# Kernel optimization log

Hardware: AMD Instinct MI355X
Metric: run time of the kernel (lower is better)

Reference implementation:

```python
import jax, jax.numpy as jnp
import numpy as np

N_USERS = 50000
N_ENTITIES = 100000
N_NODES = N_USERS + N_ENTITIES
N_EDGES = 3000000
EMB_DIM = 64
WEIGHT_SIZES = [64, 64, 32, 16]  # [emb_dim] + weight_size
BATCH = 8192
LEAKY_SLOPE = 0.2  # KGAT (TF reference) uses leaky_relu alpha=0.2
EPS = 1e-12


def setup_inputs() -> dict:
    key = jax.random.key(0)
    ks = jax.random.split(key, 24)
    inp = {}
    inp["users"] = jax.random.randint(ks[0], (BATCH,), 0, N_USERS, dtype=jnp.int32)
    inp["pos_items"] = jax.random.randint(ks[1], (BATCH,), 0, N_ENTITIES, dtype=jnp.int32)
    inp["neg_items"] = jax.random.randint(ks[2], (BATCH,), 0, N_ENTITIES, dtype=jnp.int32)
    inp["all_h"] = jax.random.randint(ks[3], (N_EDGES,), 0, N_NODES, dtype=jnp.int32)
    inp["all_t"] = jax.random.randint(ks[4], (N_EDGES,), 0, N_NODES, dtype=jnp.int32)
    inp["A_values"] = jax.random.uniform(ks[5], (N_EDGES,), dtype=jnp.float32)
    inp["user_embed"] = jax.random.normal(ks[6], (N_USERS, EMB_DIM), dtype=jnp.float32) * 0.1
    inp["entity_embed"] = jax.random.normal(ks[7], (N_ENTITIES, EMB_DIM), dtype=jnp.float32) * 0.1
    ki = 8
    for k in range(3):
        din, dout = WEIGHT_SIZES[k], WEIGHT_SIZES[k + 1]
        scale = float(np.sqrt(2.0 / (din + dout)))  # xavier-ish
        inp[f"W_gc_{k}"] = jax.random.normal(ks[ki], (din, dout), dtype=jnp.float32) * scale; ki += 1
        inp[f"b_gc_{k}"] = jax.random.normal(ks[ki], (1, dout), dtype=jnp.float32) * scale; ki += 1
        inp[f"W_bi_{k}"] = jax.random.normal(ks[ki], (din, dout), dtype=jnp.float32) * scale; ki += 1
        inp[f"b_bi_{k}"] = jax.random.normal(ks[ki], (1, dout), dtype=jnp.float32) * scale; ki += 1
    return inp


def _bi_interaction(ego, all_h, all_t, A_values, layers, n_nodes):
    # KGAT bi-interaction aggregator over edge-list sparse adjacency.
    outs = [ego]
    for (W_gc, b_gc, W_bi, b_bi) in layers:
        # sparse A @ ego : gather tails, weight by attention, scatter-add to heads
        msgs = A_values[:, None] * ego[all_t]                       # [E, d]
        side = jax.ops.segment_sum(msgs, all_h, num_segments=n_nodes)  # [N, d]
        sum_emb = jax.nn.leaky_relu((ego + side) @ W_gc + b_gc, negative_slope=LEAKY_SLOPE)
        bi_emb = jax.nn.leaky_relu((ego * side) @ W_bi + b_bi, negative_slope=LEAKY_SLOPE)
        ego = sum_emb + bi_emb
        norm = ego / jnp.maximum(jnp.linalg.norm(ego, axis=1, keepdims=True), EPS)
        outs.append(norm)
    return jnp.concatenate(outs, axis=1)  # [N, 64+64+32+16]


def reference(users, pos_items, neg_items, all_h, all_t, A_values,
              user_embed, entity_embed,
              W_gc_0, b_gc_0, W_bi_0, b_bi_0,
              W_gc_1, b_gc_1, W_bi_1, b_bi_1,
              W_gc_2, b_gc_2, W_bi_2, b_bi_2):
    n_users = user_embed.shape[0]
    n_nodes = n_users + entity_embed.shape[0]
    ego = jnp.concatenate([user_embed, entity_embed], axis=0)  # [N, 64]
    layers = [(W_gc_0, b_gc_0, W_bi_0, b_bi_0),
              (W_gc_1, b_gc_1, W_bi_1, b_bi_1),
              (W_gc_2, b_gc_2, W_bi_2, b_bi_2)]
    all_emb = _bi_interaction(ego, all_h, all_t, A_values, layers, n_nodes)
    ua, ea = all_emb[:n_users], all_emb[n_users:]
    u_e = ua[users]
    pos_i_e = ea[pos_items]
    neg_i_e = ea[neg_items]
    return (u_e, pos_i_e, neg_i_e)
```

## Files before the change

### kernel.cpp

```cpp
#include <hip/hip_runtime.h>
#include <math.h>

#define N_USERS    50000
#define N_ENTITIES 100000
#define N_NODES    150000
#define N_EDGES    3000000
#define BATCH      8192
#define SLOPE      0.2f
#define EPSF       1e-12f

#define NBUK   2344
#define CAP    1536
#define STR    2560
#define PADM   16
#define BLK_E  12288
#define NPB    ((N_EDGES + BLK_E - 1) / BLK_E)
#define PBLK   1024
#define EPT    (BLK_E / PBLK)
#define CH     4096
#define PFW    (NBUK + 1)
#define CASTB  ((N_NODES * 64 / 4 + PBLK - 1) / PBLK)

__device__ __forceinline__ unsigned f2bf(float f) {
    unsigned u = __float_as_uint(f);
    return (u + 0x7FFFu + ((u >> 16) & 1u)) >> 16;
}
__device__ __forceinline__ float bf_lo(unsigned d) { return __uint_as_float(d << 16); }
__device__ __forceinline__ float bf_hi(unsigned d) { return __uint_as_float(d); }

__global__ __launch_bounds__(PBLK)
void prep_k(const int* __restrict__ all_h, const int* __restrict__ all_t,
            const float* __restrict__ A,
            int* __restrict__ prefix, int2* __restrict__ rec_src,
            const float* __restrict__ user_emb, const float* __restrict__ ent_emb,
            unsigned short* __restrict__ ego0_bf) {
    __shared__ int pos[NBUK];
    __shared__ int wsum[PBLK / 64];
    __shared__ int2 srec[CH];

    int t = threadIdx.x;

    if (blockIdx.x >= NPB) {
        int idx = (blockIdx.x - NPB) * PBLK + t;
        const int total = N_NODES * 64 / 4;
        if (idx >= total) return;
        int ge = idx * 4;
        const float* src = (ge < N_USERS * 64) ? user_emb + ge
                                               : ent_emb + (ge - N_USERS * 64);
        float4 v = *(const float4*)src;
        ushort4 o;
        o.x = (unsigned short)f2bf(v.x);
        o.y = (unsigned short)f2bf(v.y);
        o.z = (unsigned short)f2bf(v.z);
        o.w = (unsigned short)f2bf(v.w);
        *(ushort4*)(ego0_bf + ge) = o;
        return;
    }

    for (int i = t; i < NBUK; i += PBLK) pos[i] = 0;
    __syncthreads();

    int e0 = blockIdx.x * BLK_E;
    int e1 = e0 + BLK_E; if (e1 > N_EDGES) e1 = N_EDGES;
    int tot = e1 - e0;

    int h[EPT]; int tt[EPT]; float aa[EPT];
    #pragma unroll
    for (int k = 0; k < EPT; ++k) {
        int e = e0 + k * PBLK + t;
        bool v = e < e1;
        h[k]  = v ? all_h[e] : -1;
        tt[k] = v ? all_t[e] : 0;
        aa[k] = v ? A[e] : 0.f;
    }
    #pragma unroll
    for (int k = 0; k < EPT; ++k)
        if (h[k] >= 0) atomicAdd(&pos[h[k] >> 6], 1);
    __syncthreads();

    int c[3];
    int i0 = t * 3;
    int tsum = 0;
    #pragma unroll
    for (int j = 0; j < 3; ++j) {
        int idx = i0 + j;
        c[j] = (idx < NBUK) ? pos[idx] : 0;
        tsum += c[j];
    }

    int lane = t & 63, w = t >> 6;
    int incl = tsum;
    #pragma unroll
    for (int off = 1; off < 64; off <<= 1) {
        int x = __shfl_up(incl, off, 64);
        if (lane >= off) incl += x;
    }
    if (lane == 63) wsum[w] = incl;
    __syncthreads();
    int wbase = 0;
    for (int j = 0; j < w; ++j) wbase += wsum[j];
    int excl = wbase + (incl - tsum);

    size_t prow = (size_t)blockIdx.x * PFW;
    #pragma unroll
    for (int j = 0; j < 3; ++j) {
        int idx = i0 + j;
        if (idx < NBUK) { pos[idx] = excl; prefix[prow + idx] = excl; }
        excl += c[j];
    }
    if (t == PBLK - 1) prefix[prow + NBUK] = excl;
    __syncthreads();

    int pp[EPT];
    #pragma unroll
    for (int k = 0; k < EPT; ++k)
        pp[k] = (h[k] >= 0) ? atomicAdd(&pos[h[k] >> 6], 1) : -1;

    for (int base = 0; base < tot; base += CH) {
        __syncthreads();
        int lim = tot - base; if (lim > CH) lim = CH;
        #pragma unroll
        for (int k = 0; k < EPT; ++k) {
            int s = pp[k] - base;
            if (s >= 0 && s < CH)
                srec[s] = make_int2(tt[k] | ((h[k] & 63) << 18), __float_as_int(aa[k]));
        }
        __syncthreads();
        const int4* s4 = (const int4*)srec;
        int4* d4 = (int4*)(rec_src + e0 + base);
        int lim2 = lim >> 1;
        for (int s = t; s < lim2; s += PBLK) d4[s] = s4[s];
    }
}

__global__ __launch_bounds__(256)
void local_sort_k(const int* __restrict__ prefix, const int2* __restrict__ rec_src,
                  int2* __restrict__ rec, int2* __restrict__ range) {
    __shared__ int2 sin[CAP];
    __shared__ int2 sout[STR];
    __shared__ int cnt64[64];
    __shared__ int pos64[64];
    __shared__ int sc[256];
    __shared__ int s_ptot;
    int b = blockIdx.x, t = threadIdx.x;

    if (t < 64) cnt64[t] = 0;

    int rstart = 0, n_t = 0;
    if (t < NPB) {
        const int* prow = prefix + (size_t)t * PFW + b;
        int s0 = prow[0];
        int s1 = prow[1];
        rstart = t * BLK_E + s0;
        n_t = s1 - s0;
    }
    sc[t] = n_t;
    __syncthreads();

    for (int off = 1; off < 256; off <<= 1) {
        int v = sc[t];
        int u = (t >= off) ? sc[t - off] : 0;
        __syncthreads();
        sc[t] = v + u;
        __syncthreads();
    }
    int cnt = sc[255]; if (cnt > CAP) cnt = CAP;

    if (t < NPB && n_t > 0) {
        int d = sc[t] - n_t;
        for (int j = 0; j < n_t; ++j) {
            int dj = d + j;
            if (dj >= CAP) break;
            int2 p = rec_src[rstart + j];
            sin[dj] = p;
            atomicAdd(&cnt64[(p.x >> 18) & 63], 1);
        }
    }
    __syncthreads();

    if (t < 64) {
        int v = cnt64[t];
        int pv = (v + PADM - 1) & ~(PADM - 1);
        int sum = pv;
        #pragma unroll
        for (int off = 1; off < 64; off <<= 1) {
            int x = __shfl_up(sum, off, 64);
            if (t >= off) sum += x;
        }
        pos64[t] = sum - pv;
        if (t == 63) s_ptot = sum;
    }
    __syncthreads();
    int ptot = s_ptot;

    for (int i = t; i < ptot; i += 256) sout[i] = make_int2(0, 0);
    __syncthreads();

    for (int i = t; i < cnt; i += 256) {
        int2 p = sin[i];
        int l = (p.x >> 18) & 63;
        int dst = atomicAdd(&pos64[l], 1);
        sout[dst] = make_int2(p.x & 0x3FFFF, p.y);
    }
    __syncthreads();

    for (int i = t; i < ptot; i += 256)
        rec[(size_t)b * STR + i] = sout[i];

    if (t < 64) {
        int v = cnt64[t];
        int pv = (v + PADM - 1) & ~(PADM - 1);
        int sum = pv;
        #pragma unroll
        for (int off = 1; off < 64; off <<= 1) {
            int x = __shfl_up(sum, off, 64);
            if (t >= off) sum += x;
        }
        int start = b * STR + (sum - pv);
        int node = b * 64 + t;
        if (node < N_NODES) range[node] = make_int2(start, start + pv);
    }
}

template<int DIN>
__global__ __launch_bounds__(256)
void side_k(const int2* __restrict__ range, const int2* __restrict__ rec,
            const unsigned short* __restrict__ tab, float* __restrict__ side) {
    constexpr int LPR = DIN / 8;
    constexpr int EPW = 64 / LPR;

    int w = threadIdx.x >> 6;
    int lane = threadIdx.x & 63;
    int h = blockIdx.x * 4 + w;

    int2 rg = range[h];
    int e0 = rg.x, e1 = rg.y;
    int g = lane / LPR;
    int q = lane % LPR;

    float acc[8];
    #pragma unroll
    for (int j = 0; j < 8; ++j) acc[j] = 0.f;

    int e = e0;
    for (; e + 2 * EPW <= e1; e += 2 * EPW) {
        int2 p0 = rec[e + g];
        int2 p1 = rec[e + EPW + g];
        float a0 = __int_as_float(p0.y);
        float a1 = __int_as_float(p1.y);
        uint4 d0 = *(const uint4*)(tab + (unsigned)(p0.x * DIN) + q * 8);
        uint4 d1 = *(const uint4*)(tab + (unsigned)(p1.x * DIN) + q * 8);
        acc[0] = fmaf(a0, bf_lo(d0.x), acc[0]);
        acc[1] = fmaf(a0, bf_hi(d0.x), acc[1]);
        acc[2] = fmaf(a0, bf_lo(d0.y), acc[2]);
        acc[3] = fmaf(a0, bf_hi(d0.y), acc[3]);
        acc[4] = fmaf(a0, bf_lo(d0.z), acc[4]);
        acc[5] = fmaf(a0, bf_hi(d0.z), acc[5]);
        acc[6] = fmaf(a0, bf_lo(d0.w), acc[6]);
        acc[7] = fmaf(a0, bf_hi(d0.w), acc[7]);
        acc[0] = fmaf(a1, bf_lo(d1.x), acc[0]);
        acc[1] = fmaf(a1, bf_hi(d1.x), acc[1]);
        acc[2] = fmaf(a1, bf_lo(d1.y), acc[2]);
        acc[3] = fmaf(a1, bf_hi(d1.y), acc[3]);
        acc[4] = fmaf(a1, bf_lo(d1.z), acc[4]);
        acc[5] = fmaf(a1, bf_hi(d1.z), acc[5]);
        acc[6] = fmaf(a1, bf_lo(d1.w), acc[6]);
        acc[7] = fmaf(a1, bf_hi(d1.w), acc[7]);
    }
    if (e < e1) {
        int2 p0 = rec[e + g];
        float a0 = __int_as_float(p0.y);
        uint4 d0 = *(const uint4*)(tab + (unsigned)(p0.x * DIN) + q * 8);
        acc[0] = fmaf(a0, bf_lo(d0.x), acc[0]);
        acc[1] = fmaf(a0, bf_hi(d0.x), acc[1]);
        acc[2] = fmaf(a0, bf_lo(d0.y), acc[2]);
        acc[3] = fmaf(a0, bf_hi(d0.y), acc[3]);
        acc[4] = fmaf(a0, bf_lo(d0.z), acc[4]);
        acc[5] = fmaf(a0, bf_hi(d0.z), acc[5]);
        acc[6] = fmaf(a0, bf_lo(d0.w), acc[6]);
        acc[7] = fmaf(a0, bf_hi(d0.w), acc[7]);
    }

    #pragma unroll
    for (int off = LPR; off < 64; off <<= 1)
        #pragma unroll
        for (int j = 0; j < 8; ++j) acc[j] += __shfl_xor(acc[j], off, 64);

    if (lane < LPR) {
        float* dst = side + (size_t)h * DIN + q * 8;
        *(float4*)dst       = make_float4(acc[0], acc[1], acc[2], acc[3]);
        *(float4*)(dst + 4) = make_float4(acc[4], acc[5], acc[6], acc[7]);
    }
}

template<int DIN, int DOUT, int TILE_ROWS, bool CONCAT, bool OUT_BF>
__global__ __launch_bounds__(256)
void transform_k(const unsigned short* __restrict__ ego_in,
                 const float* __restrict__ user_emb, const float* __restrict__ ent_emb,
                 const float* __restrict__ side,
                 const float* __restrict__ Wgc, const float* __restrict__ bgc,
                 const float* __restrict__ Wbi, const float* __restrict__ bbi,
                 void* __restrict__ ego_out) {
    constexpr int NG = DOUT / 8;
    constexpr int RG = 256 / NG;
    constexpr int RT = TILE_ROWS / RG;
    constexpr int STRIDE = DIN + 4;
    constexpr int KC8 = DIN / 8;

    __shared__ float sWgc[DIN * DOUT], sWbi[DIN * DOUT];
    __shared__ float sU[TILE_ROWS * STRIDE], sV[TILE_ROWS * STRIDE];

    int t = threadIdx.x;

    for (int i = t * 4; i < DIN * DOUT; i += 1024) {
        *(float4*)&sWgc[i] = *(const float4*)&Wgc[i];
        *(float4*)&sWbi[i] = *(const float4*)&Wbi[i];
    }

    int base = blockIdx.x * TILE_ROWS;
    for (int f = t; f < TILE_ROWS * KC8; f += 256) {
        int row = f / KC8, c8 = f % KC8;
        int n = base + row;
        int nc = n < N_NODES ? n : N_NODES - 1;
        float ev[8];
        if (CONCAT) {
            const float* erow = (nc < N_USERS) ? user_emb + (size_t)nc * 64
                                               : ent_emb + (size_t)(nc - N_USERS) * 64;
            float4 a = *(const float4*)(erow + c8 * 8);
            float4 b = *(const float4*)(erow + c8 * 8 + 4);
            ev[0] = a.x; ev[1] = a.y; ev[2] = a.z; ev[3] = a.w;
            ev[4] = b.x; ev[5] = b.y; ev[6] = b.z; ev[7] = b.w;
        } else {
            uint4 d = *(const uint4*)(ego_in + (size_t)nc * DIN + c8 * 8);
            ev[0] = bf_lo(d.x); ev[1] = bf_hi(d.x);
            ev[2] = bf_lo(d.y); ev[3] = bf_hi(d.y);
            ev[4] = bf_lo(d.z); ev[5] = bf_hi(d.z);
            ev[6] = bf_lo(d.w); ev[7] = bf_hi(d.w);
        }
        const float* srow = side + (size_t)nc * DIN + c8 * 8;
        float4 s0 = *(const float4*)srow;
        float4 s1 = *(const float4*)(srow + 4);
        float sv8[8] = {s0.x, s0.y, s0.z, s0.w, s1.x, s1.y, s1.z, s1.w};
        float* pu = &sU[row * STRIDE + c8 * 8];
        float* pv = &sV[row * STRIDE + c8 * 8];
        *(float4*)pu       = make_float4(ev[0] + sv8[0], ev[1] + sv8[1], ev[2] + sv8[2], ev[3] + sv8[3]);
        *(float4*)(pu + 4) = make_float4(ev[4] + sv8[4], ev[5] + sv8[5], ev[6] + sv8[6], ev[7] + sv8[7]);
        *(float4*)pv       = make_float4(ev[0] * sv8[0], ev[1] * sv8[1], ev[2] * sv8[2], ev[3] * sv8[3]);
        *(float4*)(pv + 4) = make_float4(ev[4] * sv8[4], ev[5] * sv8[5], ev[6] * sv8[6], ev[7] * sv8[7]);
    }
    __syncthreads();

    int cg = t % NG, rgi = t / NG;
    int c0 = cg * 8;
    int r0 = rgi * RT;

    float accg[RT][8], accb[RT][8];
    #pragma unroll
    for (int r = 0; r < RT; ++r)
        #pragma unroll
        for (int j = 0; j < 8; ++j) { accg[r][j] = 0.f; accb[r][j] = 0.f; }

    for (int k = 0; k < DIN; k += 4) {
        float4 u4[RT], v4[RT];
        #pragma unroll
        for (int r = 0; r < RT; ++r) {
            u4[r] = *(const float4*)&sU[(r0 + r) * STRIDE + k];
            v4[r] = *(const float4*)&sV[(r0 + r) * STRIDE + k];
        }
        #pragma unroll
        for (int kk = 0; kk < 4; ++kk) {
            float4 wg0 = *(const float4*)&sWgc[(k + kk) * DOUT + c0];
            float4 wg1 = *(const float4*)&sWgc[(k + kk) * DOUT + c0 + 4];
            float4 wb0 = *(const float4*)&sWbi[(k + kk) * DOUT + c0];
            float4 wb1 = *(const float4*)&sWbi[(k + kk) * DOUT + c0 + 4];
            #pragma unroll
            for (int r = 0; r < RT; ++r) {
                float u = ((const float*)&u4[r])[kk];
                float v = ((const float*)&v4[r])[kk];
                accg[r][0] = fmaf(u, wg0.x, accg[r][0]);
                accg[r][1] = fmaf(u, wg0.y, accg[r][1]);
                accg[r][2] = fmaf(u, wg0.z, accg[r][2]);
                accg[r][3] = fmaf(u, wg0.w, accg[r][3]);
                accg[r][4] = fmaf(u, wg1.x, accg[r][4]);
                accg[r][5] = fmaf(u, wg1.y, accg[r][5]);
                accg[r][6] = fmaf(u, wg1.z, accg[r][6]);
                accg[r][7] = fmaf(u, wg1.w, accg[r][7]);
                accb[r][0] = fmaf(v, wb0.x, accb[r][0]);
                accb[r][1] = fmaf(v, wb0.y, accb[r][1]);
                accb[r][2] = fmaf(v, wb0.z, accb[r][2]);
                accb[r][3] = fmaf(v, wb0.w, accb[r][3]);
                accb[r][4] = fmaf(v, wb1.x, accb[r][4]);
                accb[r][5] = fmaf(v, wb1.y, accb[r][5]);
                accb[r][6] = fmaf(v, wb1.z, accb[r][6]);
                accb[r][7] = fmaf(v, wb1.w, accb[r][7]);
            }
        }
    }

    float4 bg0 = *(const float4*)&bgc[c0];
    float4 bg1 = *(const float4*)&bgc[c0 + 4];
    float4 bb0 = *(const float4*)&bbi[c0];
    float4 bb1 = *(const float4*)&bbi[c0 + 4];
    float bg[8] = {bg0.x, bg0.y, bg0.z, bg0.w, bg1.x, bg1.y, bg1.z, bg1.w};
    float bb[8] = {bb0.x, bb0.y, bb0.z, bb0.w, bb1.x, bb1.y, bb1.z, bb1.w};

    #pragma unroll
    for (int r = 0; r < RT; ++r) {
        int n = base + r0 + r;
        if (n < N_NODES) {
            float o[8];
            #pragma unroll
            for (int j = 0; j < 8; ++j) {
                float gg = accg[r][j] + bg[j];
                float b2 = accb[r][j] + bb[j];
                gg = gg > 0.f ? gg : SLOPE * gg;
                b2 = b2 > 0.f ? b2 : SLOPE * b2;
                o[j] = gg + b2;
            }
            if (OUT_BF) {
                unsigned short* dst = (unsigned short*)ego_out + (size_t)n * DOUT + c0;
                uint4 wv;
                wv.x = f2bf(o[0]) | (f2bf(o[1]) << 16);
                wv.y = f2bf(o[2]) | (f2bf(o[3]) << 16);
                wv.z = f2bf(o[4]) | (f2bf(o[5]) << 16);
                wv.w = f2bf(o[6]) | (f2bf(o[7]) << 16);
                *(uint4*)dst = wv;
            } else {
                float* dst = (float*)ego_out + (size_t)n * DOUT + c0;
                *(float4*)dst       = make_float4(o[0], o[1], o[2], o[3]);
                *(float4*)(dst + 4) = make_float4(o[4], o[5], o[6], o[7]);
            }
        }
    }
}

__global__ __launch_bounds__(256)
void gather_k(const int* __restrict__ users, const int* __restrict__ pos,
              const int* __restrict__ neg,
              const float* __restrict__ user_emb, const float* __restrict__ ent_emb,
              const unsigned short* __restrict__ ego1_bf,
              const unsigned short* __restrict__ ego2_bf,
              const float* __restrict__ ego3,
              float* __restrict__ out) {
    int w = threadIdx.x >> 6;
    int lane = threadIdx.x & 63;
    int r = blockIdx.x * 4 + w;
    int which = r / BATCH;
    int i = r - which * BATCH;
    int node;
    if (which == 0)      node = users[i];
    else if (which == 1) node = N_USERS + pos[i];
    else                 node = N_USERS + neg[i];

    float* o = out + (size_t)r * 176;

    float x0 = (node < N_USERS) ? user_emb[(size_t)node * 64 + lane]
                                : ent_emb[(size_t)(node - N_USERS) * 64 + lane];
    o[lane] = x0;

    float x1 = __uint_as_float((unsigned)ego1_bf[(size_t)node * 64 + lane] << 16);
    float ss = x1 * x1;
    #pragma unroll
    for (int off = 32; off > 0; off >>= 1) ss += __shfl_xor(ss, off, 64);
    o[64 + lane] = x1 / fmaxf(sqrtf(ss), EPSF);

    float x2 = (lane < 32)
        ? __uint_as_float((unsigned)ego2_bf[(size_t)node * 32 + lane] << 16) : 0.f;
    float ss2 = x2 * x2;
    #pragma unroll
    for (int off = 32; off > 0; off >>= 1) ss2 += __shfl_xor(ss2, off, 64);
    if (lane < 32) o[128 + lane] = x2 / fmaxf(sqrtf(ss2), EPSF);

    float x3 = (lane < 16) ? ego3[(size_t)node * 16 + lane] : 0.f;
    float ss3 = x3 * x3;
    #pragma unroll
    for (int off = 32; off > 0; off >>= 1) ss3 += __shfl_xor(ss3, off, 64);
    if (lane < 16) o[160 + lane] = x3 / fmaxf(sqrtf(ss3), EPSF);
}

extern "C" void kernel_launch(void* const* d_in, const int* in_sizes, int n_in,
                              void* d_out, int out_size, void* d_ws, size_t ws_size,
                              hipStream_t stream) {
    const int*   users    = (const int*)d_in[0];
    const int*   pos      = (const int*)d_in[1];
    const int*   neg      = (const int*)d_in[2];
    const int*   all_h    = (const int*)d_in[3];
    const int*   all_t    = (const int*)d_in[4];
    const float* A        = (const float*)d_in[5];
    const float* user_emb = (const float*)d_in[6];
    const float* ent_emb  = (const float*)d_in[7];
    const float* Wgc0 = (const float*)d_in[8];
    const float* bgc0 = (const float*)d_in[9];
    const float* Wbi0 = (const float*)d_in[10];
    const float* bbi0 = (const float*)d_in[11];
    const float* Wgc1 = (const float*)d_in[12];
    const float* bgc1 = (const float*)d_in[13];
    const float* Wbi1 = (const float*)d_in[14];
    const float* bbi1 = (const float*)d_in[15];
    const float* Wgc2 = (const float*)d_in[16];
    const float* bgc2 = (const float*)d_in[17];
    const float* Wbi2 = (const float*)d_in[18];
    const float* bbi2 = (const float*)d_in[19];

    char* p = (char*)d_ws;
    int*   prefix  = (int*)p;            p += ((size_t)NPB * PFW * 4 + 255) & ~255ull;
    float* side    = (float*)p;
    int2*  rec_src = (int2*)p;           p += ((size_t)N_NODES * 64 * 4 + 255) & ~255ull;
    int2*  rec     = (int2*)p;           char* rec_base = p;
    p += ((size_t)NBUK * STR * 8 + 255) & ~255ull;
    int2*  range   = (int2*)p;           p += ((size_t)N_NODES * 8 + 255) & ~255ull;
    unsigned short* ego0_bf = (unsigned short*)p; p += ((size_t)N_NODES * 64 * 2 + 255) & ~255ull;
    unsigned short* ego1_bf = (unsigned short*)p; p += ((size_t)N_NODES * 64 * 2 + 255) & ~255ull;
    unsigned short* ego2_bf = (unsigned short*)p; p += ((size_t)N_NODES * 32 * 2 + 255) & ~255ull;
    float* ego3    = (float*)rec_base;
    float* out     = (float*)d_out;

    const int nodeBlocks = N_NODES / 4;

    prep_k<<<NPB + CASTB, PBLK, 0, stream>>>(all_h, all_t, A, prefix, rec_src,
                                             user_emb, ent_emb, ego0_bf);
    local_sort_k<<<NBUK, 256, 0, stream>>>(prefix, rec_src, rec, range);

    side_k<64><<<nodeBlocks, 256, 0, stream>>>(range, rec, ego0_bf, side);
    transform_k<64, 64, 64, true, true><<<(N_NODES + 63) / 64, 256, 0, stream>>>(
        nullptr, user_emb, ent_emb, side, Wgc0, bgc0, Wbi0, bbi0, ego1_bf);

    side_k<64><<<nodeBlocks, 256, 0, stream>>>(range, rec, ego1_bf, side);
    transform_k<64, 32, 64, false, true><<<(N_NODES + 63) / 64, 256, 0, stream>>>(
        ego1_bf, nullptr, nullptr, side, Wgc1, bgc1, Wbi1, bbi1, ego2_bf);

    side_k<32><<<nodeBlocks, 256, 0, stream>>>(range, rec, ego2_bf, side);
    transform_k<32, 16, 128, false, false><<<(N_NODES + 127) / 128, 256, 0, stream>>>(
        ego2_bf, nullptr, nullptr, side, Wgc2, bgc2, Wbi2, bbi2, ego3);

    gather_k<<<3 * BATCH / 4, 256, 0, stream>>>(
        users, pos, neg, user_emb, ent_emb, ego1_bf, ego2_bf, ego3, out);
}
```

Before: 476.6 us.

## Compute last layer only for batch nodes inside fused final gather kernel

The third-layer aggregation and transform no longer run over all 150k nodes. A fused final kernel computes that layer's sparse aggregation, linear transforms, activation and normalization only for the 3x8192 gathered batch rows. This drops one full side pass and one full transform pass over all nodes, plus the fp32 ego3 buffer. Duplicate batch nodes are recomputed, and each wave now runs a serial per-row edge loop and shuffle-based matvec.

```diff
diff --git a/kernel.cpp b/kernel.cpp
--- a/kernel.cpp
+++ b/kernel.cpp
@@ -293,14 +293,14 @@
     }
 }
 
-template<int DIN, int DOUT, int TILE_ROWS, bool CONCAT, bool OUT_BF>
+template<int DIN, int DOUT, int TILE_ROWS, bool CONCAT>
 __global__ __launch_bounds__(256)
 void transform_k(const unsigned short* __restrict__ ego_in,
                  const float* __restrict__ user_emb, const float* __restrict__ ent_emb,
                  const float* __restrict__ side,
                  const float* __restrict__ Wgc, const float* __restrict__ bgc,
                  const float* __restrict__ Wbi, const float* __restrict__ bbi,
-                 void* __restrict__ ego_out) {
+                 unsigned short* __restrict__ ego_out) {
     constexpr int NG = DOUT / 8;
     constexpr int RG = 256 / NG;
     constexpr int RT = TILE_ROWS / RG;
@@ -417,33 +417,33 @@
                 b2 = b2 > 0.f ? b2 : SLOPE * b2;
                 o[j] = gg + b2;
             }
-            if (OUT_BF) {
-                unsigned short* dst = (unsigned short*)ego_out + (size_t)n * DOUT + c0;
-                uint4 wv;
-                wv.x = f2bf(o[0]) | (f2bf(o[1]) << 16);
-                wv.y = f2bf(o[2]) | (f2bf(o[3]) << 16);
-                wv.z = f2bf(o[4]) | (f2bf(o[5]) << 16);
-                wv.w = f2bf(o[6]) | (f2bf(o[7]) << 16);
-                *(uint4*)dst = wv;
-            } else {
-                float* dst = (float*)ego_out + (size_t)n * DOUT + c0;
-                *(float4*)dst       = make_float4(o[0], o[1], o[2], o[3]);
-                *(float4*)(dst + 4) = make_float4(o[4], o[5], o[6], o[7]);
-            }
+            unsigned short* dst = ego_out + (size_t)n * DOUT + c0;
+            uint4 wv;
+            wv.x = f2bf(o[0]) | (f2bf(o[1]) << 16);
+            wv.y = f2bf(o[2]) | (f2bf(o[3]) << 16);
+            wv.z = f2bf(o[4]) | (f2bf(o[5]) << 16);
+            wv.w = f2bf(o[6]) | (f2bf(o[7]) << 16);
+            *(uint4*)dst = wv;
         }
     }
 }
 
 __global__ __launch_bounds__(256)
-void gather_k(const int* __restrict__ users, const int* __restrict__ pos,
-              const int* __restrict__ neg,
-              const float* __restrict__ user_emb, const float* __restrict__ ent_emb,
-              const unsigned short* __restrict__ ego1_bf,
-              const unsigned short* __restrict__ ego2_bf,
-              const float* __restrict__ ego3,
-              float* __restrict__ out) {
-    int w = threadIdx.x >> 6;
-    int lane = threadIdx.x & 63;
+void final_k(const int* __restrict__ users, const int* __restrict__ pos,
+             const int* __restrict__ neg,
+             const float* __restrict__ user_emb, const float* __restrict__ ent_emb,
+             const unsigned short* __restrict__ ego1_bf,
+             const unsigned short* __restrict__ ego2_bf,
+             const int2* __restrict__ range, const int2* __restrict__ rec,
+             const float* __restrict__ Wgc, const float* __restrict__ bgc,
+             const float* __restrict__ Wbi, const float* __restrict__ bbi,
+             float* __restrict__ out) {
+    __shared__ float sWgc[32 * 16], sWbi[32 * 16];
+    int t = threadIdx.x;
+    for (int i = t; i < 32 * 16; i += 256) { sWgc[i] = Wgc[i]; sWbi[i] = Wbi[i]; }
+    __syncthreads();
+
+    int w = t >> 6, lane = t & 63;
     int r = blockIdx.x * 4 + w;
     int which = r / BATCH;
     int i = r - which * BATCH;
@@ -471,11 +471,87 @@
     for (int off = 32; off > 0; off >>= 1) ss2 += __shfl_xor(ss2, off, 64);
     if (lane < 32) o[128 + lane] = x2 / fmaxf(sqrtf(ss2), EPSF);
 
-    float x3 = (lane < 16) ? ego3[(size_t)node * 16 + lane] : 0.f;
-    float ss3 = x3 * x3;
-    #pragma unroll
-    for (int off = 32; off > 0; off >>= 1) ss3 += __shfl_xor(ss3, off, 64);
-    if (lane < 16) o[160 + lane] = x3 / fmaxf(sqrtf(ss3), EPSF);
+    constexpr int LPR = 4, EPW = 16;
+    int g = lane / LPR, q = lane % LPR;
+    int2 rg = range[node];
+    int e0 = rg.x, e1 = rg.y;
+
+    float acc[8];
+    #pragma unroll
+    for (int j = 0; j < 8; ++j) acc[j] = 0.f;
+
+    int e = e0;
+    for (; e + 2 * EPW <= e1; e += 2 * EPW) {
+        int2 p0 = rec[e + g];
+        int2 p1 = rec[e + EPW + g];
+        float a0 = __int_as_float(p0.y);
+        float a1 = __int_as_float(p1.y);
+        uint4 d0 = *(const uint4*)(ego2_bf + (unsigned)(p0.x * 32) + q * 8);
+        uint4 d1 = *(const uint4*)(ego2_bf + (unsigned)(p1.x * 32) + q * 8);
+        acc[0] = fmaf(a0, bf_lo(d0.x), acc[0]);
+        acc[1] = fmaf(a0, bf_hi(d0.x), acc[1]);
+        acc[2] = fmaf(a0, bf_lo(d0.y), acc[2]);
+        acc[3] = fmaf(a0, bf_hi(d0.y), acc[3]);
+        acc[4] = fmaf(a0, bf_lo(d0.z), acc[4]);
+        acc[5] = fmaf(a0, bf_hi(d0.z), acc[5]);
+        acc[6] = fmaf(a0, bf_lo(d0.w), acc[6]);
+        acc[7] = fmaf(a0, bf_hi(d0.w), acc[7]);
+        acc[0] = fmaf(a1, bf_lo(d1.x), acc[0]);
+        acc[1] = fmaf(a1, bf_hi(d1.x), acc[1]);
+        acc[2] = fmaf(a1, bf_lo(d1.y), acc[2]);
+        acc[3] = fmaf(a1, bf_hi(d1.y), acc[3]);
+        acc[4] = fmaf(a1, bf_lo(d1.z), acc[4]);
+        acc[5] = fmaf(a1, bf_hi(d1.z), acc[5]);
+        acc[6] = fmaf(a1, bf_lo(d1.w), acc[6]);
+        acc[7] = fmaf(a1, bf_hi(d1.w), acc[7]);
+    }
+    if (e < e1) {
+        int2 p0 = rec[e + g];
+        float a0 = __int_as_float(p0.y);
+        uint4 d0 = *(const uint4*)(ego2_bf + (unsigned)(p0.x * 32) + q * 8);
+        acc[0] = fmaf(a0, bf_lo(d0.x), acc[0]);
+        acc[1] = fmaf(a0, bf_hi(d0.x), acc[1]);
+        acc[2] = fmaf(a0, bf_lo(d0.y), acc[2]);
+        acc[3] = fmaf(a0, bf_hi(d0.y), acc[3]);
+        acc[4] = fmaf(a0, bf_lo(d0.z), acc[4]);
+        acc[5] = fmaf(a0, bf_hi(d0.z), acc[5]);
+        acc[6] = fmaf(a0, bf_lo(d0.w), acc[6]);
+        acc[7] = fmaf(a0, bf_hi(d0.w), acc[7]);
+    }
+
+    #pragma unroll
+    for (int off = LPR; off < 64; off <<= 1)
+        #pragma unroll
+        for (int j = 0; j < 8; ++j) acc[j] += __shfl_xor(acc[j], off, 64);
+
+    uint4 dd = *(const uint4*)(ego2_bf + (size_t)node * 32 + q * 8);
+    float Uc[8], Vc[8];
+    {
+        float ev[8] = { bf_lo(dd.x), bf_hi(dd.x), bf_lo(dd.y), bf_hi(dd.y),
+                        bf_lo(dd.z), bf_hi(dd.z), bf_lo(dd.w), bf_hi(dd.w) };
+        #pragma unroll
+        for (int j = 0; j < 8; ++j) { Uc[j] = ev[j] + acc[j]; Vc[j] = ev[j] * acc[j]; }
+    }
+
+    if (lane < 16) {
+        float accg = 0.f, accb = 0.f;
+        #pragma unroll
+        for (int k = 0; k < 32; ++k) {
+            float u = __shfl(Uc[k & 7], k >> 3, 64);
+            float v = __shfl(Vc[k & 7], k >> 3, 64);
+            accg = fmaf(u, sWgc[k * 16 + lane], accg);
+            accb = fmaf(v, sWbi[k * 16 + lane], accb);
+        }
+        float gg = accg + bgc[lane];
+        float b2 = accb + bbi[lane];
+        gg = gg > 0.f ? gg : SLOPE * gg;
+        b2 = b2 > 0.f ? b2 : SLOPE * b2;
+        float x3 = gg + b2;
+        float ss3 = x3 * x3;
+        #pragma unroll
+        for (int off = 8; off > 0; off >>= 1) ss3 += __shfl_xor(ss3, off, 64);
+        o[160 + lane] = x3 / fmaxf(sqrtf(ss3), EPSF);
+    }
 }
 
 extern "C" void kernel_launch(void* const* d_in, const int* in_sizes, int n_in,
@@ -506,13 +582,11 @@
     int*   prefix  = (int*)p;            p += ((size_t)NPB * PFW * 4 + 255) & ~255ull;
     float* side    = (float*)p;
     int2*  rec_src = (int2*)p;           p += ((size_t)N_NODES * 64 * 4 + 255) & ~255ull;
-    int2*  rec     = (int2*)p;           char* rec_base = p;
-    p += ((size_t)NBUK * STR * 8 + 255) & ~255ull;
+    int2*  rec     = (int2*)p;           p += ((size_t)NBUK * STR * 8 + 255) & ~255ull;
     int2*  range   = (int2*)p;           p += ((size_t)N_NODES * 8 + 255) & ~255ull;
     unsigned short* ego0_bf = (unsigned short*)p; p += ((size_t)N_NODES * 64 * 2 + 255) & ~255ull;
     unsigned short* ego1_bf = (unsigned short*)p; p += ((size_t)N_NODES * 64 * 2 + 255) & ~255ull;
     unsigned short* ego2_bf = (unsigned short*)p; p += ((size_t)N_NODES * 32 * 2 + 255) & ~255ull;
-    float* ego3    = (float*)rec_base;
     float* out     = (float*)d_out;
 
     const int nodeBlocks = N_NODES / 4;
@@ -522,17 +596,14 @@
     local_sort_k<<<NBUK, 256, 0, stream>>>(prefix, rec_src, rec, range);
 
     side_k<64><<<nodeBlocks, 256, 0, stream>>>(range, rec, ego0_bf, side);
-    transform_k<64, 64, 64, true, true><<<(N_NODES + 63) / 64, 256, 0, stream>>>(
+    transform_k<64, 64, 64, true><<<(N_NODES + 63) / 64, 256, 0, stream>>>(
         nullptr, user_emb, ent_emb, side, Wgc0, bgc0, Wbi0, bbi0, ego1_bf);
 
     side_k<64><<<nodeBlocks, 256, 0, stream>>>(range, rec, ego1_bf, side);
-    transform_k<64, 32, 64, false, true><<<(N_NODES + 63) / 64, 256, 0, stream>>>(
+    transform_k<64, 32, 64, false><<<(N_NODES + 63) / 64, 256, 0, stream>>>(
         ego1_bf, nullptr, nullptr, side, Wgc1, bgc1, Wbi1, bbi1, ego2_bf);
 
-    side_k<32><<<nodeBlocks, 256, 0, stream>>>(range, rec, ego2_bf, side);
-    transform_k<32, 16, 128, false, false><<<(N_NODES + 127) / 128, 256, 0, stream>>>(
-        ego2_bf, nullptr, nullptr, side, Wgc2, bgc2, Wbi2, bbi2, ego3);
-
-    gather_k<<<3 * BATCH / 4, 256, 0, stream>>>(
-        users, pos, neg, user_emb, ent_emb, ego1_bf, ego2_bf, ego3, out);
+    final_k<<<3 * BATCH / 4, 256, 0, stream>>>(
+        users, pos, neg, user_emb, ent_emb, ego1_bf, ego2_bf,
+        range, rec, Wgc2, bgc2, Wbi2, bbi2, out);
 }
```

New measurement: 442.0 us, median of 2. -7.3%, faster.
